# Optimization experiments

Measured on AMD Instinct MI355X. Metric: run time of the kernel, lower is better.

## Reference

```python
import jax, jax.numpy as jnp
import numpy as np

N_AGENTS = 8
N_HEADS = 4
HYP = 128   # hypernet_embed
EMB = 32    # mixing_embed_dim


def _hypernet(entities, entity_mask, fc1_w, fc1_b, attn_w, out_w, out_b, fc2_w, fc2_b):
    # entities: [B, ne, ed]; entity_mask: [B, ne] (1 = masked/inactive)
    B, ne, _ = entities.shape
    hd = HYP // N_HEADS
    x1 = jax.nn.relu(entities @ fc1_w + fc1_b)                      # [B, ne, HYP]
    am = entity_mask[:, :N_AGENTS].astype(x1.dtype)                 # [B, na]
    em = entity_mask.astype(x1.dtype)                               # [B, ne]
    # attn_mask[b,i,j] = 1 - (1-am[i])*(1-em[j]): mask if agent i OR entity j inactive
    pre_mask = 1.0 - (1.0 - am)[:, :, None] * (1.0 - em)[:, None, :]  # [B, na, ne]
    # EntityAttentionLayer: agents are the queries, all entities are keys/values
    qkv = x1 @ attn_w                                               # [B, ne, 3*HYP] (no bias)
    q, k, v = jnp.split(qkv, 3, axis=-1)
    q = q[:, :N_AGENTS].reshape(B, N_AGENTS, N_HEADS, hd)
    k = k.reshape(B, ne, N_HEADS, hd)
    v = v.reshape(B, ne, N_HEADS, hd)
    scale = jnp.asarray(np.sqrt(hd), x1.dtype)
    logits = jnp.einsum('bqhd,bkhd->bhqk', q, k) / scale            # [B, H, na, ne]
    m = pre_mask[:, None, :, :]
    # masked softmax; fully-masked rows (torch: -inf -> NaN -> 0) become 0 via *(1-m)
    w = jax.nn.softmax(jnp.where(m > 0, -1e30, logits), axis=-1) * (1.0 - m)
    attn = jnp.einsum('bhqk,bkhd->bqhd', w, v).reshape(B, N_AGENTS, HYP)
    attn = attn @ out_w + out_b                                     # [B, na, HYP]
    keep = (1.0 - am)[:, :, None]                                   # zero masked agents (post_mask)
    attn = attn * keep
    x3 = (attn @ fc2_w + fc2_b) * keep                              # [B, na, EMB]
    return x3


def reference(agent_qs, entities, entity_mask, fc1_w, fc1_b, attn_w, out_w, out_b, fc2_w, fc2_b):
    bs, T, ne, ed = entities.shape
    B = bs * T
    ents = entities.reshape(B, ne, ed)
    emask = entity_mask.reshape(B, ne)
    qs = agent_qs.reshape(B, N_AGENTS)
    # 4 hypernets: 0=hyper_w_1 (matrix), 1=hyper_w_final (vector), 2=hyper_b_1 (vector), 3=V (scalar)
    outs = [_hypernet(ents, emask, fc1_w[i], fc1_b[i], attn_w[i], out_w[i],
                      out_b[i], fc2_w[i], fc2_b[i]) for i in range(4)]
    w1 = jax.nn.softmax(outs[0], axis=-1)                           # [B, na, EMB]
    b1 = outs[2].mean(axis=1)                                       # [B, EMB]
    hidden = jax.nn.elu(jnp.einsum('ba,bae->be', qs, w1) + b1)      # [B, EMB]
    w_final = jax.nn.softmax(outs[1].mean(axis=1), axis=-1)         # [B, EMB]
    v = outs[3].mean(axis=(1, 2))                                   # [B]
    y = jnp.sum(hidden * w_final, axis=-1) + v                      # [B]
    return y.reshape(bs, T, 1)


def setup_inputs() -> dict:
    key = jax.random.key(0)
    ks = jax.random.split(key, 10)
    bs, T, ne, ed = 128, 64, 16, 64
    s = 0.05
    return {
        'agent_qs': jax.random.normal(ks[0], (bs, T, N_AGENTS), jnp.float32),
        'entities': jax.random.normal(ks[1], (bs, T, ne, ed), jnp.float32),
        'entity_mask': jax.random.randint(ks[2], (bs, T, ne), 0, 2, jnp.int32),
        'fc1_w': jax.random.normal(ks[3], (4, ed, HYP), jnp.float32) * s,
        'fc1_b': jax.random.normal(ks[4], (4, HYP), jnp.float32) * s,
        'attn_w': jax.random.normal(ks[5], (4, HYP, 3 * HYP), jnp.float32) * s,
        'out_w': jax.random.normal(ks[6], (4, HYP, HYP), jnp.float32) * s,
        'out_b': jax.random.normal(ks[7], (4, HYP), jnp.float32) * s,
        'fc2_w': jax.random.normal(ks[8], (4, HYP, EMB), jnp.float32) * s,
        'fc2_b': jax.random.normal(ks[9], (4, EMB), jnp.float32) * s,
    }
```

## Files before the change

### kernel.cpp

```cpp
#include <hip/hip_runtime.h>
#include <math.h>

#define NAG 8
#define NE  16
#define ED  64
#define HYPD 128
#define QKVW 384
#define SB 4

#define X1S 132
#define KS  132
#define QS  132

#define OFF_X1    0
#define OFF_SLOG  0
#define OFF_ATTN  8448
#define OFF_K     16896
#define OFF_ATTN2 16896
#define OFF_Q     33792
#define OFF_OUT0  42240
#define OFF_MEANS 44288
#define OFF_EM    45824
#define LDS_BYTES 46080

typedef __attribute__((ext_vector_type(8))) short bf16x8;
typedef __attribute__((ext_vector_type(4))) short bf16x4;
typedef __attribute__((ext_vector_type(4))) float f32x4;

__device__ __forceinline__ short f2bf(float f) {
    union { float f; unsigned u; } c; c.f = f;
    unsigned r = (c.u + 0x7FFFu + ((c.u >> 16) & 1u)) >> 16;
    return (short)r;
}
__device__ __forceinline__ float bf2f(short s) {
    union { unsigned u; float f; } c; c.u = ((unsigned)(unsigned short)s) << 16; return c.f;
}
__device__ __forceinline__ bf16x8 ld_frag(const short* p) {
    bf16x4 lo = *(const bf16x4*)p;
    bf16x4 hi = *(const bf16x4*)(p + 16);
    return __builtin_shufflevector(lo, hi, 0, 1, 2, 3, 4, 5, 6, 7);
}

__global__ void pack_weights(const float* __restrict__ fc1_w,
                             const float* __restrict__ attn_w,
                             const float* __restrict__ out_w,
                             const float* __restrict__ fc2_w,
                             short* __restrict__ ws) {
    int gid = blockIdx.x * 256 + threadIdx.x;
    if (gid >= 608 * 64) return;
    int slot = gid >> 6, l = gid & 63;
    const float* src; int N, nt, kt;
    if (slot < 64) {
        int h = slot >> 4, f = slot & 15;
        nt = f >> 1; kt = f & 1; N = HYPD; src = fc1_w + h * ED * HYPD;
    } else if (slot < 448) {
        int s2 = slot - 64; int h = s2 / 96, f = s2 % 96;
        nt = f >> 2; kt = f & 3; N = QKVW; src = attn_w + h * HYPD * QKVW;
    } else if (slot < 576) {
        int s2 = slot - 448; int h = s2 >> 5, f = s2 & 31;
        nt = f >> 2; kt = f & 3; N = HYPD; src = out_w + h * HYPD * HYPD;
    } else {
        int s2 = slot - 576; int h = s2 >> 3, f = s2 & 7;
        nt = f >> 2; kt = f & 3; N = 32; src = fc2_w + h * HYPD * 32;
    }
    int rg = l >> 4, lc = l & 15;
    bf16x8 fr;
    #pragma unroll
    for (int j = 0; j < 8; ++j) {
        int k = kt * 32 + 4 * rg + (j & 3) + 16 * (j >> 2);
        fr[j] = f2bf(src[k * N + nt * 16 + lc]);
    }
    ((bf16x8*)ws)[slot * 64 + l] = fr;
}

__global__ __launch_bounds__(256, 2) void flexq_mfma(
    const float* __restrict__ agent_qs,
    const float* __restrict__ entities,
    const int*   __restrict__ entity_mask,
    const float* __restrict__ fc1_b,
    const float* __restrict__ out_b,
    const float* __restrict__ fc2_b,
    const short* __restrict__ wfrag,
    float* __restrict__ out, int B)
{
    __shared__ __align__(16) char smem[LDS_BYTES];
    short* x1    = (short*)(smem + OFF_X1);
    float* slog  = (float*)(smem + OFF_SLOG);
    short* attn  = (short*)(smem + OFF_ATTN);
    short* k     = (short*)(smem + OFF_K);
    short* attn2 = (short*)(smem + OFF_ATTN2);
    short* q     = (short*)(smem + OFF_Q);
    short* out0  = (short*)(smem + OFF_OUT0);
    float* means = (float*)(smem + OFF_MEANS);
    float* em    = (float*)(smem + OFF_EM);

    const int tid = threadIdx.x;
    const int l = tid & 63, w = tid >> 6;
    const int rg = l >> 4, lc = l & 15;
    const int b4 = blockIdx.x * SB;
    const bf16x8* WF = (const bf16x8*)wfrag;

    if (tid < 64)
        em[tid] = (entity_mask[(size_t)b4 * NE + tid] != 0) ? 1.0f : 0.0f;

    bf16x8 aent[2][4];
    #pragma unroll
    for (int kt = 0; kt < 2; ++kt)
        #pragma unroll
        for (int mt = 0; mt < 4; ++mt) {
            const float* ap = entities + ((size_t)(b4 + mt) * NE + lc) * ED + kt * 32 + rg * 4;
            float4 lo = *(const float4*)ap;
            float4 hi = *(const float4*)(ap + 16);
            bf16x8 af;
            af[0]=f2bf(lo.x); af[1]=f2bf(lo.y); af[2]=f2bf(lo.z); af[3]=f2bf(lo.w);
            af[4]=f2bf(hi.x); af[5]=f2bf(hi.y); af[6]=f2bf(hi.z); af[7]=f2bf(hi.w);
            aent[kt][mt] = af;
        }
    __syncthreads();

    for (int i = 0; i < 4; ++i) {
        {
            f32x4 acc[4][2];
            #pragma unroll
            for (int mt = 0; mt < 4; ++mt) {
                acc[mt][0] = (f32x4){0.f,0.f,0.f,0.f};
                acc[mt][1] = (f32x4){0.f,0.f,0.f,0.f};
            }
            __builtin_amdgcn_s_setprio(1);
            #pragma unroll
            for (int kt = 0; kt < 2; ++kt) {
                bf16x8 b0 = WF[(i*16 + (2*w+0)*2 + kt)*64 + l];
                bf16x8 b1 = WF[(i*16 + (2*w+1)*2 + kt)*64 + l];
                #pragma unroll
                for (int mt = 0; mt < 4; ++mt) {
                    acc[mt][0] = __builtin_amdgcn_mfma_f32_16x16x32_bf16(aent[kt][mt], b0, acc[mt][0], 0,0,0);
                    acc[mt][1] = __builtin_amdgcn_mfma_f32_16x16x32_bf16(aent[kt][mt], b1, acc[mt][1], 0,0,0);
                }
            }
            __builtin_amdgcn_s_setprio(0);
            float bias0 = fc1_b[i*HYPD + 32*w + lc];
            float bias1 = fc1_b[i*HYPD + 32*w + 16 + lc];
            #pragma unroll
            for (int mt = 0; mt < 4; ++mt)
                #pragma unroll
                for (int r = 0; r < 4; ++r) {
                    int row = 16*mt + 4*rg + r;
                    x1[row*X1S + 32*w + lc]      = f2bf(fmaxf(acc[mt][0][r] + bias0, 0.f));
                    x1[row*X1S + 32*w + 16 + lc] = f2bf(fmaxf(acc[mt][1][r] + bias1, 0.f));
                }
        }
        __syncthreads();

        f32x4 accv[4][2];
        {
            f32x4 acc[4][3];
            #pragma unroll
            for (int mt = 0; mt < 4; ++mt)
                #pragma unroll
                for (int n = 0; n < 3; ++n) acc[mt][n] = (f32x4){0.f,0.f,0.f,0.f};
            __builtin_amdgcn_s_setprio(1);
            #pragma unroll
            for (int kt = 0; kt < 4; ++kt) {
                bf16x8 b0 = WF[(64 + i*96 + (w +  0)*4 + kt)*64 + l];
                bf16x8 b1 = WF[(64 + i*96 + (w +  4)*4 + kt)*64 + l];
                bf16x8 b2 = WF[(64 + i*96 + (w +  8)*4 + kt)*64 + l];
                #pragma unroll
                for (int mt = 0; mt < 4; ++mt) {
                    bf16x8 a = ld_frag(x1 + (16*mt + lc)*X1S + kt*32 + rg*4);
                    acc[mt][0] = __builtin_amdgcn_mfma_f32_16x16x32_bf16(a, b0, acc[mt][0], 0,0,0);
                    acc[mt][1] = __builtin_amdgcn_mfma_f32_16x16x32_bf16(a, b1, acc[mt][1], 0,0,0);
                    acc[mt][2] = __builtin_amdgcn_mfma_f32_16x16x32_bf16(a, b2, acc[mt][2], 0,0,0);
                }
            }
            __builtin_amdgcn_s_setprio(0);
            #pragma unroll
            for (int mt = 0; mt < 4; ++mt)
                #pragma unroll
                for (int r = 0; r < 4; ++r) {
                    if (rg < 2) {
                        q[(mt*NAG + 4*rg + r)*QS + (w+0)*16 + lc] = f2bf(acc[mt][0][r]);
                        q[(mt*NAG + 4*rg + r)*QS + (w+4)*16 + lc] = f2bf(acc[mt][1][r]);
                    }
                    k[(16*mt + 4*rg + r)*KS + w*16 + lc] = f2bf(acc[mt][2][r]);
                }
        }
        {
            f32x4 acck[4];
            #pragma unroll
            for (int mt = 0; mt < 4; ++mt) {
                acck[mt] = (f32x4){0.f,0.f,0.f,0.f};
                accv[mt][0] = (f32x4){0.f,0.f,0.f,0.f};
                accv[mt][1] = (f32x4){0.f,0.f,0.f,0.f};
            }
            __builtin_amdgcn_s_setprio(1);
            #pragma unroll
            for (int kt = 0; kt < 4; ++kt) {
                bf16x8 b0 = WF[(64 + i*96 + (w + 12)*4 + kt)*64 + l];
                bf16x8 b1 = WF[(64 + i*96 + (w + 16)*4 + kt)*64 + l];
                bf16x8 b2 = WF[(64 + i*96 + (w + 20)*4 + kt)*64 + l];
                #pragma unroll
                for (int mt = 0; mt < 4; ++mt) {
                    bf16x8 a = ld_frag(x1 + (16*mt + lc)*X1S + kt*32 + rg*4);
                    acck[mt]    = __builtin_amdgcn_mfma_f32_16x16x32_bf16(a, b0, acck[mt], 0,0,0);
                    accv[mt][0] = __builtin_amdgcn_mfma_f32_16x16x32_bf16(a, b1, accv[mt][0], 0,0,0);
                    accv[mt][1] = __builtin_amdgcn_mfma_f32_16x16x32_bf16(a, b2, accv[mt][1], 0,0,0);
                }
            }
            __builtin_amdgcn_s_setprio(0);
            #pragma unroll
            for (int mt = 0; mt < 4; ++mt)
                #pragma unroll
                for (int r = 0; r < 4; ++r)
                    k[(16*mt + 4*rg + r)*KS + (w+4)*16 + lc] = f2bf(acck[mt][r]);
        }
        __syncthreads();

        {
            __builtin_amdgcn_s_setprio(1);
            #pragma unroll
            for (int pp = 0; pp < 4; ++pp) {
                int p = 4*w + pp, s = p >> 2, h = p & 3;
                bf16x8 a  = ld_frag(q + (s*NAG + (lc & 7))*QS + h*32 + rg*4);
                bf16x8 bb = ld_frag(k + (s*NE  + lc)*KS       + h*32 + rg*4);
                f32x4 acc = (f32x4){0.f,0.f,0.f,0.f};
                acc = __builtin_amdgcn_mfma_f32_16x16x32_bf16(a, bb, acc, 0,0,0);
                if (rg < 2) {
                    #pragma unroll
                    for (int r = 0; r < 4; ++r)
                        slog[((s*4 + h)*NAG + 4*rg + r)*16 + lc] = acc[r] * 0.17677669529663687f;
                }
            }
            __builtin_amdgcn_s_setprio(0);
        }
        __syncthreads();

        if (tid < 128) {
            int s = tid >> 5, h = (tid >> 3) & 3, qi = tid & 7;
            float am = em[s*NE + qi];
            float* rowp = slog + ((s*4 + h)*NAG + qi)*16;
            float mx = -3.0e38f; bool any = false;
            #pragma unroll
            for (int kk = 0; kk < NE; ++kk)
                if (em[s*NE + kk] == 0.f) { any = true; mx = fmaxf(mx, rowp[kk]); }
            if (am != 0.f || !any) {
                #pragma unroll
                for (int kk = 0; kk < NE; ++kk) rowp[kk] = 0.f;
            } else {
                float eb[NE]; float sum = 0.f;
                #pragma unroll
                for (int kk = 0; kk < NE; ++kk) {
                    float e = (em[s*NE + kk] == 0.f) ? __expf(rowp[kk] - mx) : 0.f;
                    eb[kk] = e; sum += e;
                }
                float inv = 1.f / sum;
                #pragma unroll
                for (int kk = 0; kk < NE; ++kk) rowp[kk] = eb[kk] * inv;
            }
        }
        __syncthreads();

        {
            __builtin_amdgcn_s_setprio(1);
            #pragma unroll
            for (int vt = 0; vt < 2; ++vt) {
                int c = w + 4*vt;
                int h = c >> 1;
                #pragma unroll
                for (int mt = 0; mt < 4; ++mt) {
                    f32x4 pw = *(const f32x4*)(slog + ((mt*4 + h)*NAG + (lc & 7))*16 + 4*rg);
                    bf16x8 a;
                    a[0]=f2bf(pw[0]); a[1]=f2bf(pw[1]); a[2]=f2bf(pw[2]); a[3]=f2bf(pw[3]);
                    a[4]=0; a[5]=0; a[6]=0; a[7]=0;
                    bf16x8 bb;
                    bb[0]=f2bf(accv[mt][vt][0]); bb[1]=f2bf(accv[mt][vt][1]);
                    bb[2]=f2bf(accv[mt][vt][2]); bb[3]=f2bf(accv[mt][vt][3]);
                    bb[4]=0; bb[5]=0; bb[6]=0; bb[7]=0;
                    f32x4 po = (f32x4){0.f,0.f,0.f,0.f};
                    po = __builtin_amdgcn_mfma_f32_16x16x32_bf16(a, bb, po, 0,0,0);
                    if (rg < 2) {
                        #pragma unroll
                        for (int r = 0; r < 4; ++r)
                            attn[(mt*NAG + 4*rg + r)*X1S + c*16 + lc] = f2bf(po[r]);
                    }
                }
            }
            __builtin_amdgcn_s_setprio(0);
        }
        __syncthreads();

        {
            f32x4 acc[2][2];
            #pragma unroll
            for (int mt = 0; mt < 2; ++mt) {
                acc[mt][0] = (f32x4){0.f,0.f,0.f,0.f};
                acc[mt][1] = (f32x4){0.f,0.f,0.f,0.f};
            }
            __builtin_amdgcn_s_setprio(1);
            #pragma unroll
            for (int kt = 0; kt < 4; ++kt) {
                bf16x8 b0 = WF[(448 + i*32 + (2*w+0)*4 + kt)*64 + l];
                bf16x8 b1 = WF[(448 + i*32 + (2*w+1)*4 + kt)*64 + l];
                #pragma unroll
                for (int mt = 0; mt < 2; ++mt) {
                    bf16x8 a = ld_frag(attn + (16*mt + lc)*X1S + kt*32 + rg*4);
                    acc[mt][0] = __builtin_amdgcn_mfma_f32_16x16x32_bf16(a, b0, acc[mt][0], 0,0,0);
                    acc[mt][1] = __builtin_amdgcn_mfma_f32_16x16x32_bf16(a, b1, acc[mt][1], 0,0,0);
                }
            }
            __builtin_amdgcn_s_setprio(0);
            float bias0 = out_b[i*HYPD + 32*w + lc];
            float bias1 = out_b[i*HYPD + 32*w + 16 + lc];
            #pragma unroll
            for (int mt = 0; mt < 2; ++mt)
                #pragma unroll
                for (int r = 0; r < 4; ++r) {
                    int row = 16*mt + 4*rg + r;
                    float keep = 1.f - em[(row >> 3)*NE + (row & 7)];
                    attn2[row*X1S + 32*w + lc]      = f2bf((acc[mt][0][r] + bias0) * keep);
                    attn2[row*X1S + 32*w + 16 + lc] = f2bf((acc[mt][1][r] + bias1) * keep);
                }
        }
        __syncthreads();

        {
            int mt = w >> 1, nt = w & 1;
            f32x4 acc = (f32x4){0.f,0.f,0.f,0.f};
            __builtin_amdgcn_s_setprio(1);
            #pragma unroll
            for (int kt = 0; kt < 4; ++kt) {
                bf16x8 a = ld_frag(attn2 + (16*mt + lc)*X1S + kt*32 + rg*4);
                bf16x8 bfr = WF[(576 + i*8 + nt*4 + kt)*64 + l];
                acc = __builtin_amdgcn_mfma_f32_16x16x32_bf16(a, bfr, acc, 0,0,0);
            }
            __builtin_amdgcn_s_setprio(0);
            float bias = fc2_b[i*32 + nt*16 + lc];
            float vals[4];
            #pragma unroll
            for (int r = 0; r < 4; ++r) {
                int row = 16*mt + 4*rg + r;
                float keep = 1.f - em[(row >> 3)*NE + (row & 7)];
                vals[r] = (acc[r] + bias) * keep;
            }
            if (i == 0) {
                #pragma unroll
                for (int r = 0; r < 4; ++r)
                    out0[(16*mt + 4*rg + r)*32 + nt*16 + lc] = f2bf(vals[r]);
            } else {
                float ps = vals[0] + vals[1] + vals[2] + vals[3];
                ps += __shfl_xor(ps, 16);
                if ((rg & 1) == 0) {
                    int s = 2*mt + (rg >> 1);
                    means[(i-1)*128 + s*32 + nt*16 + lc] = ps;
                }
            }
        }
        __syncthreads();
    }

    if (l < 32) {
        int s = w, c = l;
        float s1 = means[0*128 + s*32 + c] * 0.125f;
        float b1 = means[1*128 + s*32 + c] * 0.125f;
        float vsum = means[2*128 + s*32 + c];

        float hid = 0.f;
        #pragma unroll
        for (int a = 0; a < NAG; ++a) {
            float x = bf2f(out0[(s*NAG + a)*32 + c]);
            float mx = x;
            #pragma unroll
            for (int m = 16; m >= 1; m >>= 1) mx = fmaxf(mx, __shfl_xor(mx, m, 32));
            float e = __expf(x - mx);
            float sum = e;
            #pragma unroll
            for (int m = 16; m >= 1; m >>= 1) sum += __shfl_xor(sum, m, 32);
            float qsv = agent_qs[(size_t)(b4 + s)*NAG + a];
            hid += qsv * (e / sum);
        }
        hid += b1;
        hid = (hid > 0.f) ? hid : expm1f(hid);

        float mx = s1;
        #pragma unroll
        for (int m = 16; m >= 1; m >>= 1) mx = fmaxf(mx, __shfl_xor(mx, m, 32));
        float e = __expf(s1 - mx);
        float ss = e;
        #pragma unroll
        for (int m = 16; m >= 1; m >>= 1) ss += __shfl_xor(ss, m, 32);
        float wf = e / ss;

        float red = hid * wf + vsum * (1.f / 256.f);
        #pragma unroll
        for (int m = 16; m >= 1; m >>= 1) red += __shfl_xor(red, m, 32);
        if (c == 0) out[b4 + s] = red;
    }
}

#define QKVP 388
#define NTHR 384
__device__ __forceinline__ float4 f4load(const float* p) { return *reinterpret_cast<const float4*>(p); }
__device__ __forceinline__ void f4store(float* p, const float4& v) { *reinterpret_cast<float4*>(p) = v; }
__device__ __forceinline__ void f4fma(float4& a, float s, const float4& w) {
    a.x += s * w.x; a.y += s * w.y; a.z += s * w.z; a.w += s * w.w;
}

__global__ __launch_bounds__(NTHR) void flexq_fp32(
    const float* __restrict__ agent_qs, const float* __restrict__ entities,
    const int* __restrict__ entity_mask, const float* __restrict__ fc1_w,
    const float* __restrict__ fc1_b, const float* __restrict__ attn_w,
    const float* __restrict__ out_w, const float* __restrict__ out_b,
    const float* __restrict__ fc2_w, const float* __restrict__ fc2_b,
    float* __restrict__ out)
{
    const int b = blockIdx.x, tid = threadIdx.x;
    __shared__ float s_ent[NE][ED];
    __shared__ float s_x1t[HYPD][NE];
    __shared__ float s_qkv[NE][QKVP];
    __shared__ float s_w[4][NAG][NE];
    __shared__ float s_attn[NAG][HYPD];
    __shared__ float s_attnout[NAG][HYPD];
    __shared__ float s_outs[4][NAG][32];
    __shared__ float s_mask[NE];
    __shared__ float s_qs[NAG];

    const float* ent = entities + (size_t)b * NE * ED;
    for (int o = tid; o < NE * ED; o += NTHR) s_ent[o >> 6][o & 63] = ent[o];
    if (tid < NE) s_mask[tid] = (entity_mask[(size_t)b * NE + tid] != 0) ? 1.0f : 0.0f;
    if (tid < NAG) s_qs[tid] = agent_qs[(size_t)b * NAG + tid];
    __syncthreads();

    for (int i = 0; i < 4; ++i) {
        {
            const float* W1 = fc1_w + i * ED * HYPD;
            const float* B1 = fc1_b + i * HYPD;
            for (int o4 = tid; o4 < 512; o4 += NTHR) {
                int e = o4 >> 5, j = (o4 & 31) * 4;
                float4 acc = f4load(B1 + j);
                for (int d = 0; d < ED; ++d) { float x = s_ent[e][d]; f4fma(acc, x, f4load(W1 + d * HYPD + j)); }
                s_x1t[j+0][e] = fmaxf(acc.x, 0.f); s_x1t[j+1][e] = fmaxf(acc.y, 0.f);
                s_x1t[j+2][e] = fmaxf(acc.z, 0.f); s_x1t[j+3][e] = fmaxf(acc.w, 0.f);
            }
        }
        __syncthreads();
        {
            const float* W2 = attn_w + i * HYPD * QKVW;
            int j = (tid % 96) * 4, e0 = (tid / 96) * 4;
            float4 a0 = {0,0,0,0}, a1 = {0,0,0,0}, a2 = {0,0,0,0}, a3 = {0,0,0,0};
            for (int d = 0; d < HYPD; ++d) {
                float4 wv = f4load(W2 + d * QKVW + j);
                float4 x = f4load(&s_x1t[d][e0]);
                f4fma(a0, x.x, wv); f4fma(a1, x.y, wv); f4fma(a2, x.z, wv); f4fma(a3, x.w, wv);
            }
            f4store(&s_qkv[e0+0][j], a0); f4store(&s_qkv[e0+1][j], a1);
            f4store(&s_qkv[e0+2][j], a2); f4store(&s_qkv[e0+3][j], a3);
        }
        __syncthreads();
        {
            const float inv_scale = 0.17677669529663687f;
            for (int o = tid; o < 512; o += NTHR) {
                int h = o >> 7, qi = (o >> 4) & 7, kk = o & 15;
                const float* qp = &s_qkv[qi][h * 32];
                const float* kp = &s_qkv[kk][HYPD + h * 32];
                float s = 0.f;
                #pragma unroll
                for (int d4 = 0; d4 < 8; ++d4) {
                    float4 qv = f4load(qp + 4 * d4), kv2 = f4load(kp + 4 * d4);
                    s += qv.x*kv2.x + qv.y*kv2.y + qv.z*kv2.z + qv.w*kv2.w;
                }
                s_w[h][qi][kk] = s * inv_scale;
            }
        }
        __syncthreads();
        if (tid < 32) {
            int h = tid >> 3, qi = tid & 7;
            float am = s_mask[qi];
            float mx = -3.0e38f; bool any = false;
            #pragma unroll
            for (int kk = 0; kk < NE; ++kk)
                if (s_mask[kk] == 0.f) { any = true; mx = fmaxf(mx, s_w[h][qi][kk]); }
            if (am != 0.f || !any) {
                #pragma unroll
                for (int kk = 0; kk < NE; ++kk) s_w[h][qi][kk] = 0.f;
            } else {
                float eb[NE]; float sum = 0.f;
                #pragma unroll
                for (int kk = 0; kk < NE; ++kk) {
                    float e = (s_mask[kk] == 0.f) ? __expf(s_w[h][qi][kk] - mx) : 0.f;
                    eb[kk] = e; sum += e;
                }
                float inv = 1.f / sum;
                #pragma unroll
                for (int kk = 0; kk < NE; ++kk) s_w[h][qi][kk] = eb[kk] * inv;
            }
        }
        __syncthreads();
        if (tid < 256) {
            int qi = tid >> 5, j = (tid & 31) * 4, h = j >> 5, d0 = j & 31;
            float4 acc = {0,0,0,0};
            #pragma unroll
            for (int kk = 0; kk < NE; ++kk) f4fma(acc, s_w[h][qi][kk], f4load(&s_qkv[kk][2*HYPD + h*32 + d0]));
            f4store(&s_attn[qi][j], acc);
        }
        __syncthreads();
        if (tid < 256) {
            const float* W3 = out_w + i * HYPD * HYPD;
            const float* B3 = out_b + i * HYPD;
            int qi = tid >> 5, j = (tid & 31) * 4;
            float4 acc = f4load(B3 + j);
            for (int d = 0; d < HYPD; ++d) f4fma(acc, s_attn[qi][d], f4load(W3 + d * HYPD + j));
            float keep = 1.f - s_mask[qi];
            acc.x *= keep; acc.y *= keep; acc.z *= keep; acc.w *= keep;
            f4store(&s_attnout[qi][j], acc);
        }
        __syncthreads();
        if (tid < 64) {
            const float* W4 = fc2_w + i * HYPD * 32;
            const float* B4 = fc2_b + i * 32;
            int qi = tid >> 3, c = (tid & 7) * 4;
            float4 acc = f4load(B4 + c);
            for (int d = 0; d < HYPD; ++d) f4fma(acc, s_attnout[qi][d], f4load(W4 + d * 32 + c));
            float keep = 1.f - s_mask[qi];
            acc.x *= keep; acc.y *= keep; acc.z *= keep; acc.w *= keep;
            f4store(&s_outs[i][qi][c], acc);
        }
        __syncthreads();
    }

    if (tid < 32) {
        const int c = tid;
        float b1 = 0.f, s1 = 0.f, vs = 0.f;
        #pragma unroll
        for (int qi = 0; qi < NAG; ++qi) {
            b1 += s_outs[2][qi][c]; s1 += s_outs[1][qi][c]; vs += s_outs[3][qi][c];
        }
        b1 *= 0.125f; s1 *= 0.125f;
        float hid = 0.f;
        #pragma unroll
        for (int a = 0; a < NAG; ++a) {
            float x = s_outs[0][a][c];
            float mx = x;
            #pragma unroll
            for (int m = 16; m >= 1; m >>= 1) mx = fmaxf(mx, __shfl_xor(mx, m, 32));
            float e = __expf(x - mx);
            float sm = e;
            #pragma unroll
            for (int m = 16; m >= 1; m >>= 1) sm += __shfl_xor(sm, m, 32);
            hid += s_qs[a] * (e / sm);
        }
        hid += b1;
        hid = (hid > 0.f) ? hid : expm1f(hid);
        float mx = s1;
        #pragma unroll
        for (int m = 16; m >= 1; m >>= 1) mx = fmaxf(mx, __shfl_xor(mx, m, 32));
        float e = __expf(s1 - mx);
        float ssum = e;
        #pragma unroll
        for (int m = 16; m >= 1; m >>= 1) ssum += __shfl_xor(ssum, m, 32);
        float wf = e / ssum;
        float red = hid * wf + vs * (1.f / 256.f);
        #pragma unroll
        for (int m = 16; m >= 1; m >>= 1) red += __shfl_xor(red, m, 32);
        if (tid == 0) out[b] = red;
    }
}

extern "C" void kernel_launch(void* const* d_in, const int* in_sizes, int n_in,
                              void* d_out, int out_size, void* d_ws, size_t ws_size,
                              hipStream_t stream) {
    const float* agent_qs    = (const float*)d_in[0];
    const float* entities    = (const float*)d_in[1];
    const int*   entity_mask = (const int*)  d_in[2];
    const float* fc1_w       = (const float*)d_in[3];
    const float* fc1_b       = (const float*)d_in[4];
    const float* attn_w      = (const float*)d_in[5];
    const float* out_w       = (const float*)d_in[6];
    const float* out_b       = (const float*)d_in[7];
    const float* fc2_w       = (const float*)d_in[8];
    const float* fc2_b       = (const float*)d_in[9];
    float* out = (float*)d_out;

    const int B = in_sizes[0] / NAG;

    if (ws_size >= (size_t)(608 * 1024) && (B % SB) == 0) {
        pack_weights<<<152, 256, 0, stream>>>(fc1_w, attn_w, out_w, fc2_w, (short*)d_ws);
        flexq_mfma<<<B / SB, 256, 0, stream>>>(agent_qs, entities, entity_mask,
                                               fc1_b, out_b, fc2_b,
                                               (const short*)d_ws, out, B);
    } else {
        flexq_fp32<<<B, NTHR, 0, stream>>>(agent_qs, entities, entity_mask,
                                           fc1_w, fc1_b, attn_w, out_w, out_b,
                                           fc2_w, fc2_b, out);
    }
}
```

Measured before the change: 189.0 us.

## Process two samples per block with two hypernets per iteration

Each block now handles 2 samples instead of 4 and runs two hypernets at once in each of 2 loop iterations, instead of one hypernet per iteration over 4 iterations. The MFMA tiles still fill the same 4-slot layout, now indexed by (hypernet, sample) pairs. The aim is twice as many blocks for better GPU occupancy, and half as many block-wide barrier phases per block, with a slightly smaller LDS footprint. The cost is that each block loads twice as many weight fragments per sample, so weight reuse across samples drops.

```diff
diff --git a/kernel.cpp b/kernel.cpp
--- a/kernel.cpp
+++ b/kernel.cpp
@@ -6,7 +6,7 @@
 #define ED  64
 #define HYPD 128
 #define QKVW 384
-#define SB 4
+#define SB 2
 
 #define X1S 132
 #define KS  132
@@ -19,9 +19,9 @@
 #define OFF_ATTN2 16896
 #define OFF_Q     33792
 #define OFF_OUT0  42240
-#define OFF_MEANS 44288
-#define OFF_EM    45824
-#define LDS_BYTES 46080
+#define OFF_MEANS 43264
+#define OFF_EM    44032
+#define LDS_BYTES 44160
 
 typedef __attribute__((ext_vector_type(8))) short bf16x8;
 typedef __attribute__((ext_vector_type(4))) short bf16x4;
@@ -97,57 +97,66 @@
     const int tid = threadIdx.x;
     const int l = tid & 63, w = tid >> 6;
     const int rg = l >> 4, lc = l & 15;
-    const int b4 = blockIdx.x * SB;
+    const int b2 = blockIdx.x * SB;
     const bf16x8* WF = (const bf16x8*)wfrag;
 
-    if (tid < 64)
-        em[tid] = (entity_mask[(size_t)b4 * NE + tid] != 0) ? 1.0f : 0.0f;
-
-    bf16x8 aent[2][4];
+    if (tid < 32)
+        em[tid] = (entity_mask[(size_t)b2 * NE + tid] != 0) ? 1.0f : 0.0f;
+
+    bf16x8 aent[2][2];
     #pragma unroll
     for (int kt = 0; kt < 2; ++kt)
         #pragma unroll
-        for (int mt = 0; mt < 4; ++mt) {
-            const float* ap = entities + ((size_t)(b4 + mt) * NE + lc) * ED + kt * 32 + rg * 4;
+        for (int s = 0; s < 2; ++s) {
+            const float* ap = entities + ((size_t)(b2 + s) * NE + lc) * ED + kt * 32 + rg * 4;
             float4 lo = *(const float4*)ap;
             float4 hi = *(const float4*)(ap + 16);
             bf16x8 af;
             af[0]=f2bf(lo.x); af[1]=f2bf(lo.y); af[2]=f2bf(lo.z); af[3]=f2bf(lo.w);
             af[4]=f2bf(hi.x); af[5]=f2bf(hi.y); af[6]=f2bf(hi.z); af[7]=f2bf(hi.w);
-            aent[kt][mt] = af;
+            aent[kt][s] = af;
         }
     __syncthreads();
 
-    for (int i = 0; i < 4; ++i) {
+    for (int i = 0; i < 2; ++i) {
         {
             f32x4 acc[4][2];
             #pragma unroll
-            for (int mt = 0; mt < 4; ++mt) {
-                acc[mt][0] = (f32x4){0.f,0.f,0.f,0.f};
-                acc[mt][1] = (f32x4){0.f,0.f,0.f,0.f};
+            for (int v = 0; v < 4; ++v) {
+                acc[v][0] = (f32x4){0.f,0.f,0.f,0.f};
+                acc[v][1] = (f32x4){0.f,0.f,0.f,0.f};
             }
             __builtin_amdgcn_s_setprio(1);
             #pragma unroll
-            for (int kt = 0; kt < 2; ++kt) {
-                bf16x8 b0 = WF[(i*16 + (2*w+0)*2 + kt)*64 + l];
-                bf16x8 b1 = WF[(i*16 + (2*w+1)*2 + kt)*64 + l];
-                #pragma unroll
-                for (int mt = 0; mt < 4; ++mt) {
-                    acc[mt][0] = __builtin_amdgcn_mfma_f32_16x16x32_bf16(aent[kt][mt], b0, acc[mt][0], 0,0,0);
-                    acc[mt][1] = __builtin_amdgcn_mfma_f32_16x16x32_bf16(aent[kt][mt], b1, acc[mt][1], 0,0,0);
-                }
-            }
+            for (int kt = 0; kt < 2; ++kt)
+                #pragma unroll
+                for (int j = 0; j < 2; ++j) {
+                    int hyp = 2*i + j;
+                    bf16x8 b0 = WF[(hyp*16 + (2*w+0)*2 + kt)*64 + l];
+                    bf16x8 b1 = WF[(hyp*16 + (2*w+1)*2 + kt)*64 + l];
+                    #pragma unroll
+                    for (int s = 0; s < 2; ++s) {
+                        int v = j*2 + s;
+                        acc[v][0] = __builtin_amdgcn_mfma_f32_16x16x32_bf16(aent[kt][s], b0, acc[v][0], 0,0,0);
+                        acc[v][1] = __builtin_amdgcn_mfma_f32_16x16x32_bf16(aent[kt][s], b1, acc[v][1], 0,0,0);
+                    }
+                }
             __builtin_amdgcn_s_setprio(0);
-            float bias0 = fc1_b[i*HYPD + 32*w + lc];
-            float bias1 = fc1_b[i*HYPD + 32*w + 16 + lc];
-            #pragma unroll
-            for (int mt = 0; mt < 4; ++mt)
-                #pragma unroll
-                for (int r = 0; r < 4; ++r) {
-                    int row = 16*mt + 4*rg + r;
-                    x1[row*X1S + 32*w + lc]      = f2bf(fmaxf(acc[mt][0][r] + bias0, 0.f));
-                    x1[row*X1S + 32*w + 16 + lc] = f2bf(fmaxf(acc[mt][1][r] + bias1, 0.f));
-                }
+            #pragma unroll
+            for (int j = 0; j < 2; ++j) {
+                float bias0 = fc1_b[(2*i+j)*HYPD + 32*w + lc];
+                float bias1 = fc1_b[(2*i+j)*HYPD + 32*w + 16 + lc];
+                #pragma unroll
+                for (int s = 0; s < 2; ++s) {
+                    int v = j*2 + s;
+                    #pragma unroll
+                    for (int r = 0; r < 4; ++r) {
+                        int row = 16*v + 4*rg + r;
+                        x1[row*X1S + 32*w + lc]      = f2bf(fmaxf(acc[v][0][r] + bias0, 0.f));
+                        x1[row*X1S + 32*w + 16 + lc] = f2bf(fmaxf(acc[v][1][r] + bias1, 0.f));
+                    }
+                }
+            }
         }
         __syncthreads();
 
@@ -155,63 +164,71 @@
         {
             f32x4 acc[4][3];
             #pragma unroll
-            for (int mt = 0; mt < 4; ++mt)
-                #pragma unroll
-                for (int n = 0; n < 3; ++n) acc[mt][n] = (f32x4){0.f,0.f,0.f,0.f};
+            for (int v = 0; v < 4; ++v)
+                #pragma unroll
+                for (int n = 0; n < 3; ++n) acc[v][n] = (f32x4){0.f,0.f,0.f,0.f};
             __builtin_amdgcn_s_setprio(1);
             #pragma unroll
-            for (int kt = 0; kt < 4; ++kt) {
-                bf16x8 b0 = WF[(64 + i*96 + (w +  0)*4 + kt)*64 + l];
-                bf16x8 b1 = WF[(64 + i*96 + (w +  4)*4 + kt)*64 + l];
-                bf16x8 b2 = WF[(64 + i*96 + (w +  8)*4 + kt)*64 + l];
-                #pragma unroll
-                for (int mt = 0; mt < 4; ++mt) {
-                    bf16x8 a = ld_frag(x1 + (16*mt + lc)*X1S + kt*32 + rg*4);
-                    acc[mt][0] = __builtin_amdgcn_mfma_f32_16x16x32_bf16(a, b0, acc[mt][0], 0,0,0);
-                    acc[mt][1] = __builtin_amdgcn_mfma_f32_16x16x32_bf16(a, b1, acc[mt][1], 0,0,0);
-                    acc[mt][2] = __builtin_amdgcn_mfma_f32_16x16x32_bf16(a, b2, acc[mt][2], 0,0,0);
-                }
-            }
+            for (int kt = 0; kt < 4; ++kt)
+                #pragma unroll
+                for (int j = 0; j < 2; ++j) {
+                    int hyp = 2*i + j;
+                    bf16x8 b0 = WF[(64 + hyp*96 + (w +  0)*4 + kt)*64 + l];
+                    bf16x8 b1 = WF[(64 + hyp*96 + (w +  4)*4 + kt)*64 + l];
+                    bf16x8 b2 = WF[(64 + hyp*96 + (w +  8)*4 + kt)*64 + l];
+                    #pragma unroll
+                    for (int s = 0; s < 2; ++s) {
+                        int v = j*2 + s;
+                        bf16x8 a = ld_frag(x1 + (16*v + lc)*X1S + kt*32 + rg*4);
+                        acc[v][0] = __builtin_amdgcn_mfma_f32_16x16x32_bf16(a, b0, acc[v][0], 0,0,0);
+                        acc[v][1] = __builtin_amdgcn_mfma_f32_16x16x32_bf16(a, b1, acc[v][1], 0,0,0);
+                        acc[v][2] = __builtin_amdgcn_mfma_f32_16x16x32_bf16(a, b2, acc[v][2], 0,0,0);
+                    }
+                }
             __builtin_amdgcn_s_setprio(0);
             #pragma unroll
-            for (int mt = 0; mt < 4; ++mt)
+            for (int v = 0; v < 4; ++v)
                 #pragma unroll
                 for (int r = 0; r < 4; ++r) {
                     if (rg < 2) {
-                        q[(mt*NAG + 4*rg + r)*QS + (w+0)*16 + lc] = f2bf(acc[mt][0][r]);
-                        q[(mt*NAG + 4*rg + r)*QS + (w+4)*16 + lc] = f2bf(acc[mt][1][r]);
+                        q[(v*NAG + 4*rg + r)*QS + (w+0)*16 + lc] = f2bf(acc[v][0][r]);
+                        q[(v*NAG + 4*rg + r)*QS + (w+4)*16 + lc] = f2bf(acc[v][1][r]);
                     }
-                    k[(16*mt + 4*rg + r)*KS + w*16 + lc] = f2bf(acc[mt][2][r]);
+                    k[(16*v + 4*rg + r)*KS + w*16 + lc] = f2bf(acc[v][2][r]);
                 }
         }
         {
             f32x4 acck[4];
             #pragma unroll
-            for (int mt = 0; mt < 4; ++mt) {
-                acck[mt] = (f32x4){0.f,0.f,0.f,0.f};
-                accv[mt][0] = (f32x4){0.f,0.f,0.f,0.f};
-                accv[mt][1] = (f32x4){0.f,0.f,0.f,0.f};
+            for (int v = 0; v < 4; ++v) {
+                acck[v] = (f32x4){0.f,0.f,0.f,0.f};
+                accv[v][0] = (f32x4){0.f,0.f,0.f,0.f};
+                accv[v][1] = (f32x4){0.f,0.f,0.f,0.f};
             }
             __builtin_amdgcn_s_setprio(1);
             #pragma unroll
-            for (int kt = 0; kt < 4; ++kt) {
-                bf16x8 b0 = WF[(64 + i*96 + (w + 12)*4 + kt)*64 + l];
-                bf16x8 b1 = WF[(64 + i*96 + (w + 16)*4 + kt)*64 + l];
-                bf16x8 b2 = WF[(64 + i*96 + (w + 20)*4 + kt)*64 + l];
-                #pragma unroll
-                for (int mt = 0; mt < 4; ++mt) {
-                    bf16x8 a = ld_frag(x1 + (16*mt + lc)*X1S + kt*32 + rg*4);
-                    acck[mt]    = __builtin_amdgcn_mfma_f32_16x16x32_bf16(a, b0, acck[mt], 0,0,0);
-                    accv[mt][0] = __builtin_amdgcn_mfma_f32_16x16x32_bf16(a, b1, accv[mt][0], 0,0,0);
-                    accv[mt][1] = __builtin_amdgcn_mfma_f32_16x16x32_bf16(a, b2, accv[mt][1], 0,0,0);
-                }
-            }
+            for (int kt = 0; kt < 4; ++kt)
+                #pragma unroll
+                for (int j = 0; j < 2; ++j) {
+                    int hyp = 2*i + j;
+                    bf16x8 b0 = WF[(64 + hyp*96 + (w + 12)*4 + kt)*64 + l];
+                    bf16x8 b1 = WF[(64 + hyp*96 + (w + 16)*4 + kt)*64 + l];
+                    bf16x8 b2 = WF[(64 + hyp*96 + (w + 20)*4 + kt)*64 + l];
+                    #pragma unroll
+                    for (int s = 0; s < 2; ++s) {
+                        int v = j*2 + s;
+                        bf16x8 a = ld_frag(x1 + (16*v + lc)*X1S + kt*32 + rg*4);
+                        acck[v]    = __builtin_amdgcn_mfma_f32_16x16x32_bf16(a, b0, acck[v], 0,0,0);
+                        accv[v][0] = __builtin_amdgcn_mfma_f32_16x16x32_bf16(a, b1, accv[v][0], 0,0,0);
+                        accv[v][1] = __builtin_amdgcn_mfma_f32_16x16x32_bf16(a, b2, accv[v][1], 0,0,0);
+                    }
+                }
             __builtin_amdgcn_s_setprio(0);
             #pragma unroll
-            for (int mt = 0; mt < 4; ++mt)
+            for (int v = 0; v < 4; ++v)
                 #pragma unroll
                 for (int r = 0; r < 4; ++r)
-                    k[(16*mt + 4*rg + r)*KS + (w+4)*16 + lc] = f2bf(acck[mt][r]);
+                    k[(16*v + 4*rg + r)*KS + (w+4)*16 + lc] = f2bf(acck[v][r]);
         }
         __syncthreads();
 
@@ -219,15 +236,15 @@
             __builtin_amdgcn_s_setprio(1);
             #pragma unroll
             for (int pp = 0; pp < 4; ++pp) {
-                int p = 4*w + pp, s = p >> 2, h = p & 3;
-                bf16x8 a  = ld_frag(q + (s*NAG + (lc & 7))*QS + h*32 + rg*4);
-                bf16x8 bb = ld_frag(k + (s*NE  + lc)*KS       + h*32 + rg*4);
+                int p = 4*w + pp, v = p >> 2, h = p & 3;
+                bf16x8 a  = ld_frag(q + (v*NAG + (lc & 7))*QS + h*32 + rg*4);
+                bf16x8 bb = ld_frag(k + (v*NE  + lc)*KS       + h*32 + rg*4);
                 f32x4 acc = (f32x4){0.f,0.f,0.f,0.f};
                 acc = __builtin_amdgcn_mfma_f32_16x16x32_bf16(a, bb, acc, 0,0,0);
                 if (rg < 2) {
                     #pragma unroll
                     for (int r = 0; r < 4; ++r)
-                        slog[((s*4 + h)*NAG + 4*rg + r)*16 + lc] = acc[r] * 0.17677669529663687f;
+                        slog[((v*4 + h)*NAG + 4*rg + r)*16 + lc] = acc[r] * 0.17677669529663687f;
                 }
             }
             __builtin_amdgcn_s_setprio(0);
@@ -235,9 +252,10 @@
         __syncthreads();
 
         if (tid < 128) {
-            int s = tid >> 5, h = (tid >> 3) & 3, qi = tid & 7;
+            int v = tid >> 5, h = (tid >> 3) & 3, qi = tid & 7;
+            int s = v & 1;
             float am = em[s*NE + qi];
-            float* rowp = slog + ((s*4 + h)*NAG + qi)*16;
+            float* rowp = slog + ((v*4 + h)*NAG + qi)*16;
             float mx = -3.0e38f; bool any = false;
             #pragma unroll
             for (int kk = 0; kk < NE; ++kk)
@@ -266,21 +284,21 @@
                 int c = w + 4*vt;
                 int h = c >> 1;
                 #pragma unroll
-                for (int mt = 0; mt < 4; ++mt) {
-                    f32x4 pw = *(const f32x4*)(slog + ((mt*4 + h)*NAG + (lc & 7))*16 + 4*rg);
+                for (int v = 0; v < 4; ++v) {
+                    f32x4 pw = *(const f32x4*)(slog + ((v*4 + h)*NAG + (lc & 7))*16 + 4*rg);
                     bf16x8 a;
                     a[0]=f2bf(pw[0]); a[1]=f2bf(pw[1]); a[2]=f2bf(pw[2]); a[3]=f2bf(pw[3]);
                     a[4]=0; a[5]=0; a[6]=0; a[7]=0;
                     bf16x8 bb;
-                    bb[0]=f2bf(accv[mt][vt][0]); bb[1]=f2bf(accv[mt][vt][1]);
-                    bb[2]=f2bf(accv[mt][vt][2]); bb[3]=f2bf(accv[mt][vt][3]);
+                    bb[0]=f2bf(accv[v][vt][0]); bb[1]=f2bf(accv[v][vt][1]);
+                    bb[2]=f2bf(accv[v][vt][2]); bb[3]=f2bf(accv[v][vt][3]);
                     bb[4]=0; bb[5]=0; bb[6]=0; bb[7]=0;
                     f32x4 po = (f32x4){0.f,0.f,0.f,0.f};
                     po = __builtin_amdgcn_mfma_f32_16x16x32_bf16(a, bb, po, 0,0,0);
                     if (rg < 2) {
                         #pragma unroll
                         for (int r = 0; r < 4; ++r)
-                            attn[(mt*NAG + 4*rg + r)*X1S + c*16 + lc] = f2bf(po[r]);
+                            attn[(v*NAG + 4*rg + r)*X1S + c*16 + lc] = f2bf(po[r]);
                     }
                 }
             }
@@ -291,77 +309,79 @@
         {
             f32x4 acc[2][2];
             #pragma unroll
-            for (int mt = 0; mt < 2; ++mt) {
-                acc[mt][0] = (f32x4){0.f,0.f,0.f,0.f};
-                acc[mt][1] = (f32x4){0.f,0.f,0.f,0.f};
+            for (int j = 0; j < 2; ++j) {
+                acc[j][0] = (f32x4){0.f,0.f,0.f,0.f};
+                acc[j][1] = (f32x4){0.f,0.f,0.f,0.f};
             }
             __builtin_amdgcn_s_setprio(1);
             #pragma unroll
-            for (int kt = 0; kt < 4; ++kt) {
-                bf16x8 b0 = WF[(448 + i*32 + (2*w+0)*4 + kt)*64 + l];
-                bf16x8 b1 = WF[(448 + i*32 + (2*w+1)*4 + kt)*64 + l];
-                #pragma unroll
-                for (int mt = 0; mt < 2; ++mt) {
-                    bf16x8 a = ld_frag(attn + (16*mt + lc)*X1S + kt*32 + rg*4);
-                    acc[mt][0] = __builtin_amdgcn_mfma_f32_16x16x32_bf16(a, b0, acc[mt][0], 0,0,0);
-                    acc[mt][1] = __builtin_amdgcn_mfma_f32_16x16x32_bf16(a, b1, acc[mt][1], 0,0,0);
-                }
-            }
+            for (int kt = 0; kt < 4; ++kt)
+                #pragma unroll
+                for (int j = 0; j < 2; ++j) {
+                    int hyp = 2*i + j;
+                    bf16x8 b0 = WF[(448 + hyp*32 + (2*w+0)*4 + kt)*64 + l];
+                    bf16x8 b1 = WF[(448 + hyp*32 + (2*w+1)*4 + kt)*64 + l];
+                    bf16x8 a = ld_frag(attn + (16*j + lc)*X1S + kt*32 + rg*4);
+                    acc[j][0] = __builtin_amdgcn_mfma_f32_16x16x32_bf16(a, b0, acc[j][0], 0,0,0);
+                    acc[j][1] = __builtin_amdgcn_mfma_f32_16x16x32_bf16(a, b1, acc[j][1], 0,0,0);
+                }
             __builtin_amdgcn_s_setprio(0);
-            float bias0 = out_b[i*HYPD + 32*w + lc];
-            float bias1 = out_b[i*HYPD + 32*w + 16 + lc];
-            #pragma unroll
-            for (int mt = 0; mt < 2; ++mt)
+            #pragma unroll
+            for (int j = 0; j < 2; ++j) {
+                float bias0 = out_b[(2*i+j)*HYPD + 32*w + lc];
+                float bias1 = out_b[(2*i+j)*HYPD + 32*w + 16 + lc];
                 #pragma unroll
                 for (int r = 0; r < 4; ++r) {
-                    int row = 16*mt + 4*rg + r;
-                    float keep = 1.f - em[(row >> 3)*NE + (row & 7)];
-                    attn2[row*X1S + 32*w + lc]      = f2bf((acc[mt][0][r] + bias0) * keep);
-                    attn2[row*X1S + 32*w + 16 + lc] = f2bf((acc[mt][1][r] + bias1) * keep);
-                }
-        }
-        __syncthreads();
-
-        {
-            int mt = w >> 1, nt = w & 1;
+                    int lr = 4*rg + r;
+                    float keep = 1.f - em[(lr >> 3)*NE + (lr & 7)];
+                    attn2[(16*j + lr)*X1S + 32*w + lc]      = f2bf((acc[j][0][r] + bias0) * keep);
+                    attn2[(16*j + lr)*X1S + 32*w + 16 + lc] = f2bf((acc[j][1][r] + bias1) * keep);
+                }
+            }
+        }
+        __syncthreads();
+
+        {
+            int j = w >> 1, nt = w & 1;
+            int hyp = 2*i + j;
             f32x4 acc = (f32x4){0.f,0.f,0.f,0.f};
             __builtin_amdgcn_s_setprio(1);
             #pragma unroll
             for (int kt = 0; kt < 4; ++kt) {
-                bf16x8 a = ld_frag(attn2 + (16*mt + lc)*X1S + kt*32 + rg*4);
-                bf16x8 bfr = WF[(576 + i*8 + nt*4 + kt)*64 + l];
+                bf16x8 a = ld_frag(attn2 + (16*j + lc)*X1S + kt*32 + rg*4);
+                bf16x8 bfr = WF[(576 + hyp*8 + nt*4 + kt)*64 + l];
                 acc = __builtin_amdgcn_mfma_f32_16x16x32_bf16(a, bfr, acc, 0,0,0);
             }
             __builtin_amdgcn_s_setprio(0);
-            float bias = fc2_b[i*32 + nt*16 + lc];
+            float bias = fc2_b[hyp*32 + nt*16 + lc];
             float vals[4];
             #pragma unroll
             for (int r = 0; r < 4; ++r) {
-                int row = 16*mt + 4*rg + r;
-                float keep = 1.f - em[(row >> 3)*NE + (row & 7)];
+                int lr = 4*rg + r;
+                float keep = 1.f - em[(lr >> 3)*NE + (lr & 7)];
                 vals[r] = (acc[r] + bias) * keep;
             }
-            if (i == 0) {
+            if (hyp == 0) {
                 #pragma unroll
                 for (int r = 0; r < 4; ++r)
-                    out0[(16*mt + 4*rg + r)*32 + nt*16 + lc] = f2bf(vals[r]);
+                    out0[(4*rg + r)*32 + nt*16 + lc] = f2bf(vals[r]);
             } else {
                 float ps = vals[0] + vals[1] + vals[2] + vals[3];
                 ps += __shfl_xor(ps, 16);
                 if ((rg & 1) == 0) {
-                    int s = 2*mt + (rg >> 1);
-                    means[(i-1)*128 + s*32 + nt*16 + lc] = ps;
+                    int s = rg >> 1;
+                    means[(hyp-1)*64 + s*32 + nt*16 + lc] = ps;
                 }
             }
         }
         __syncthreads();
     }
 
-    if (l < 32) {
+    if (w < 2 && l < 32) {
         int s = w, c = l;
-        float s1 = means[0*128 + s*32 + c] * 0.125f;
-        float b1 = means[1*128 + s*32 + c] * 0.125f;
-        float vsum = means[2*128 + s*32 + c];
+        float s1 = means[0*64 + s*32 + c] * 0.125f;
+        float b1 = means[1*64 + s*32 + c] * 0.125f;
+        float vsum = means[2*64 + s*32 + c];
 
         float hid = 0.f;
         #pragma unroll
@@ -374,7 +394,7 @@
             float sum = e;
             #pragma unroll
             for (int m = 16; m >= 1; m >>= 1) sum += __shfl_xor(sum, m, 32);
-            float qsv = agent_qs[(size_t)(b4 + s)*NAG + a];
+            float qsv = agent_qs[(size_t)(b2 + s)*NAG + a];
             hid += qsv * (e / sum);
         }
         hid += b1;
@@ -392,7 +412,7 @@
         float red = hid * wf + vsum * (1.f / 256.f);
         #pragma unroll
         for (int m = 16; m >= 1; m >>= 1) red += __shfl_xor(red, m, 32);
-        if (c == 0) out[b4 + s] = red;
+        if (c == 0) out[b2 + s] = red;
     }
 }
 
```

New measurement: 221.2 us. +17.1%, slower.
